# Optimization experiments

Measured on AMD Instinct MI355X. Metric: run time of the kernel, lower is better.

The kernel has to match this reference:

```python
import jax, jax.numpy as jnp
import numpy as np

MAX_SIZE = 650   # hard-coded node count in the original module
HIDDEN = 512     # hidden_dim
BATCH = 512      # batch_size (conv4 out channels)
IN_DIM = 512
N_EDGES = 150000


def _segment_softmax(e, dst, n):
    # torch_geometric.utils.softmax over destination-node segments
    m = jax.ops.segment_max(e, dst, num_segments=n)
    ex = jnp.exp(e - m[dst])
    s = jax.ops.segment_sum(ex, dst, num_segments=n)
    return ex / (s[dst] + 1e-16)


def _gat_conv(x, src, dst, W, a_src, a_dst, b, n, neg_slope=0.2):
    # PyG GATConv, heads=1, edge_dim=None (edge_attr ignored)
    h = x @ W                            # [n, out]
    al_s = h @ a_src                     # [n] per-node source attention logit
    al_d = h @ a_dst                     # [n] per-node dest attention logit
    e = jax.nn.leaky_relu(al_s[src] + al_d[dst], neg_slope)   # [E]
    alpha = _segment_softmax(e, dst, n)                        # [E]
    out = jax.ops.segment_sum(alpha[:, None] * h[src], dst, num_segments=n)
    return out + b


def setup_inputs() -> dict:
    key = jax.random.key(0)
    ks = jax.random.split(key, 12)
    inp = {
        "x_s": jax.random.normal(ks[0], (400, IN_DIM), jnp.float32),
        "x_t": jax.random.normal(ks[1], (250, IN_DIM), jnp.float32),
        "edge_index": jax.random.randint(ks[2], (2, N_EDGES), 0, MAX_SIZE, dtype=jnp.int32),
        "distances": jax.random.uniform(ks[3], (N_EDGES,), jnp.float32),
        "batch": jnp.zeros((MAX_SIZE,), jnp.int32),
        "W1": jax.random.normal(ks[4], (IN_DIM, HIDDEN), jnp.float32) / np.sqrt(IN_DIM).astype(np.float32),
        "a_src1": jax.random.normal(ks[5], (HIDDEN,), jnp.float32) * 0.1,
        "a_dst1": jax.random.normal(ks[6], (HIDDEN,), jnp.float32) * 0.1,
        "b1": jnp.zeros((HIDDEN,), jnp.float32),
        "W4": jax.random.normal(ks[7], (HIDDEN, BATCH), jnp.float32) / np.sqrt(HIDDEN).astype(np.float32),
        "a_src4": jax.random.normal(ks[8], (BATCH,), jnp.float32) * 0.1,
        "a_dst4": jax.random.normal(ks[9], (BATCH,), jnp.float32) * 0.1,
        "b4": jnp.zeros((BATCH,), jnp.float32),
        "fc_w": jax.random.normal(ks[10], (1, MAX_SIZE), jnp.float32) / np.sqrt(MAX_SIZE).astype(np.float32),
        "fc_b": jnp.zeros((1,), jnp.float32),
    }
    return inp


def reference(x_s, x_t, edge_index, distances, batch,
              W1, a_src1, a_dst1, b1, W4, a_src4, a_dst4, b4, fc_w, fc_b):
    # distances (edge_attr) and batch are unpacked but unused, as in the
    # original (GATConv with edge_dim=None ignores edge_attr).
    x = jnp.concatenate([x_s, x_t], axis=0)
    pad_n = max(MAX_SIZE - x.shape[0], 0)
    x = jnp.pad(x, ((0, pad_n), (0, 0)))            # [650, IN_DIM]
    # add_self_loops=True (PyG GATConv default)
    loop = jnp.arange(MAX_SIZE, dtype=edge_index.dtype)
    src = jnp.concatenate([edge_index[0], loop])
    dst = jnp.concatenate([edge_index[1], loop])
    x = _gat_conv(x, src, dst, W1, a_src1, a_dst1, b1, MAX_SIZE)
    x = jax.nn.relu(x)
    x = _gat_conv(x, src, dst, W4, a_src4, a_dst4, b4, MAX_SIZE)
    x = jax.nn.leaky_relu(x, 0.01)                  # [650, BATCH]
    x = x.reshape(BATCH, MAX_SIZE)                  # torch .view semantics (no transpose)
    x = x @ fc_w.T + fc_b                           # [BATCH, 1]
    x = x.squeeze()[None, :]                        # [1, BATCH]
    return jax.nn.sigmoid(x)
```

## Files before the change

### kernel.cpp

```cpp
#include <hip/hip_runtime.h>
#include <math.h>

#define N_NODES 650
#define DIM     512
#define E_RAW   150000
#define E_TOT   150650

#define BM 32
#define BN 64
#define BK 32
#define KC 128
#define NZ (DIM / KC)
#define CH 1024

__global__ __launch_bounds__(256)
void gemm_hp(const float* __restrict__ A, const float* __restrict__ Axt,
             const float* __restrict__ B, float* __restrict__ P,
             int M, int a_mode) {
    __shared__ float Ast[BK][BM + 2];
    __shared__ float Bs[BK][BN];
    int t  = threadIdx.x;
    int tx = t & 15, ty = t >> 4;
    int row0 = blockIdx.y * BM, col0 = blockIdx.x * BN;
    int kbase = blockIdx.z * KC;
    float acc[2][4] = {};

    for (int kb = kbase; kb < kbase + KC; kb += BK) {
        {
            int m  = t >> 3;
            int kq = (t & 7) * 4;
            int gr = row0 + m, gk = kb + kq;
            float4 v = make_float4(0.f, 0.f, 0.f, 0.f);
            if (gr < M) {
                const float* rowp;
                if (a_mode == 1)
                    rowp = (gr < 400) ? (A + (size_t)gr * DIM) : (Axt + (size_t)(gr - 400) * DIM);
                else
                    rowp = A + (size_t)gr * DIM;
                v = *(const float4*)(rowp + gk);
            }
            Ast[kq + 0][m] = v.x;
            Ast[kq + 1][m] = v.y;
            Ast[kq + 2][m] = v.z;
            Ast[kq + 3][m] = v.w;
        }
        {
            int n4 = (t & 15) * 4;
            #pragma unroll
            for (int p = 0; p < 2; p++) {
                int kk = (t >> 4) + p * 16;
                *(float4*)&Bs[kk][n4] = *(const float4*)&B[(size_t)(kb + kk) * DIM + col0 + n4];
            }
        }
        __syncthreads();
        #pragma unroll
        for (int kk = 0; kk < BK; kk++) {
            float2 a2 = *(const float2*)&Ast[kk][ty * 2];
            float4 b4 = *(const float4*)&Bs[kk][tx * 4];
            acc[0][0] += a2.x * b4.x; acc[0][1] += a2.x * b4.y;
            acc[0][2] += a2.x * b4.z; acc[0][3] += a2.x * b4.w;
            acc[1][0] += a2.y * b4.x; acc[1][1] += a2.y * b4.y;
            acc[1][2] += a2.y * b4.z; acc[1][3] += a2.y * b4.w;
        }
        __syncthreads();
    }

    float* Cout = P + (size_t)blockIdx.z * N_NODES * DIM;
    int gc0 = col0 + tx * 4;
    #pragma unroll
    for (int i = 0; i < 2; i++) {
        int gr = row0 + ty * 2 + i;
        if (gr < M)
            *(float4*)&Cout[(size_t)gr * DIM + gc0] =
                make_float4(acc[i][0], acc[i][1], acc[i][2], acc[i][3]);
    }
}

__global__ __launch_bounds__(256)
void reduce_logits(const float* __restrict__ P,
                   const float* __restrict__ asrc, const float* __restrict__ adst,
                   float* __restrict__ h, float* __restrict__ als, float* __restrict__ ald) {
    __shared__ float red[8];
    const size_t S = (size_t)N_NODES * DIM;
    int r = blockIdx.x, t = threadIdx.x;
    size_t base = (size_t)r * DIM;
    float v0 = 0.f, v1 = 0.f;
    #pragma unroll
    for (int z = 0; z < NZ; z++) {
        v0 += P[z * S + base + t];
        v1 += P[z * S + base + t + 256];
    }
    h[base + t]       = v0;
    h[base + t + 256] = v1;
    float ps = v0 * asrc[t] + v1 * asrc[t + 256];
    float pd = v0 * adst[t] + v1 * adst[t + 256];
    #pragma unroll
    for (int o = 32; o > 0; o >>= 1) {
        ps += __shfl_down(ps, o);
        pd += __shfl_down(pd, o);
    }
    if ((t & 63) == 0) { red[t >> 6] = ps; red[4 + (t >> 6)] = pd; }
    __syncthreads();
    if (t == 0) als[r] = red[0] + red[1] + red[2] + red[3];
    if (t == 1) ald[r] = red[4] + red[5] + red[6] + red[7];
}

__global__ __launch_bounds__(256)
void hist_kernel(const int* __restrict__ ei, int* __restrict__ cnt) {
    __shared__ int h[N_NODES];
    for (int l = threadIdx.x; l < N_NODES; l += 256) h[l] = 0;
    __syncthreads();
    for (int i = blockIdx.x * 256 + threadIdx.x; i < E_TOT; i += gridDim.x * 256) {
        int d = (i < E_RAW) ? ei[E_RAW + i] : i - E_RAW;
        atomicAdd(&h[d], 1);
    }
    __syncthreads();
    for (int l = threadIdx.x; l < N_NODES; l += 256) {
        int v = h[l];
        if (v) atomicAdd(&cnt[l], v);
    }
}

__global__ __launch_bounds__(1024)
void scan_kernel(const int* __restrict__ cnt, int* __restrict__ rowptr,
                 int* __restrict__ cursor) {
    __shared__ int buf[1024];
    int t = threadIdx.x;
    buf[t] = (t < N_NODES) ? cnt[t] : 0;
    __syncthreads();
    #pragma unroll
    for (int o = 1; o < 1024; o <<= 1) {
        int v = (t >= o) ? buf[t - o] : 0;
        __syncthreads();
        buf[t] += v;
        __syncthreads();
    }
    if (t < N_NODES) {
        int excl = (t == 0) ? 0 : buf[t - 1];
        rowptr[t] = excl;
        cursor[t] = excl;
    }
    if (t == 0) rowptr[N_NODES] = buf[N_NODES - 1];
}

__global__ __launch_bounds__(256)
void scatter_kernel(const int* __restrict__ ei, int* __restrict__ cursor,
                    int* __restrict__ ssrc) {
    int i = blockIdx.x * 256 + threadIdx.x;
    if (i >= E_TOT) return;
    int s, d;
    if (i < E_RAW) { s = ei[i]; d = ei[E_RAW + i]; }
    else           { s = d = i - E_RAW; }
    int pos = atomicAdd(&cursor[d], 1);
    ssrc[pos] = s;
}

__global__ __launch_bounds__(256)
void spmm_kernel(const int* __restrict__ rowptr, const int* __restrict__ ssrc,
                 const float* __restrict__ als, const float* __restrict__ ald,
                 const float* __restrict__ h, const float* __restrict__ bias,
                 float slope, float* __restrict__ outm) {
    __shared__ int   sS[CH];
    __shared__ float sE[CH];
    __shared__ float red[4];
    int d = blockIdx.x;
    int t = threadIdx.x;
    int c = blockIdx.y * 256 + t;
    int r0 = rowptr[d], r1 = rowptr[d + 1];
    int deg = r1 - r0;
    float aldd = ald[d];
    float acc = 0.f, psum = 0.f;

    for (int cb = 0; cb < deg; cb += CH) {
        int n = min(CH, deg - cb);
        __syncthreads();
        for (int l = t; l < n; l += 256) {
            int s = ssrc[r0 + cb + l];
            float v = als[s] + aldd;
            v = v > 0.f ? v : 0.2f * v;
            float ex = __expf(v);
            sS[l] = s;
            sE[l] = ex;
            psum += ex;
        }
        __syncthreads();
        int e = 0;
        for (; e + 4 <= n; e += 4) {
            int   s0 = sS[e],   s1 = sS[e+1], s2 = sS[e+2], s3 = sS[e+3];
            float e0 = sE[e],   e1 = sE[e+1], e2 = sE[e+2], e3 = sE[e+3];
            float x0 = h[(size_t)s0 * DIM + c];
            float x1 = h[(size_t)s1 * DIM + c];
            float x2 = h[(size_t)s2 * DIM + c];
            float x3 = h[(size_t)s3 * DIM + c];
            acc += e0 * x0 + e1 * x1 + e2 * x2 + e3 * x3;
        }
        for (; e < n; e++)
            acc += sE[e] * h[(size_t)sS[e] * DIM + c];
    }

    #pragma unroll
    for (int o = 32; o > 0; o >>= 1) psum += __shfl_down(psum, o);
    if ((t & 63) == 0) red[t >> 6] = psum;
    __syncthreads();
    float sum = red[0] + red[1] + red[2] + red[3];
    float v = acc / (sum + 1e-16f) + bias[c];
    v = v > 0.f ? v : slope * v;
    outm[(size_t)d * DIM + c] = v;
}

__global__ void final_kernel(const float* __restrict__ o2,
                             const float* __restrict__ fcw,
                             const float* __restrict__ fcb,
                             float* __restrict__ out) {
    int b = blockIdx.x * 4 + (threadIdx.x >> 6);
    int lane = threadIdx.x & 63;
    if (b >= 512) return;
    float s = 0.f;
    for (int i = lane; i < N_NODES; i += 64)
        s += o2[b * N_NODES + i] * fcw[i];
    #pragma unroll
    for (int o = 32; o > 0; o >>= 1) s += __shfl_down(s, o);
    if (lane == 0) out[b] = 1.f / (1.f + expf(-(s + fcb[0])));
}

extern "C" void kernel_launch(void* const* d_in, const int* in_sizes, int n_in,
                              void* d_out, int out_size, void* d_ws, size_t ws_size,
                              hipStream_t stream) {
    const float* x_s   = (const float*)d_in[0];
    const float* x_t   = (const float*)d_in[1];
    const int*   ei    = (const int*)d_in[2];
    const float* W1    = (const float*)d_in[5];
    const float* asrc1 = (const float*)d_in[6];
    const float* adst1 = (const float*)d_in[7];
    const float* b1    = (const float*)d_in[8];
    const float* W4    = (const float*)d_in[9];
    const float* asrc4 = (const float*)d_in[10];
    const float* adst4 = (const float*)d_in[11];
    const float* b4    = (const float*)d_in[12];
    const float* fcw   = (const float*)d_in[13];
    const float* fcb   = (const float*)d_in[14];
    float* out = (float*)d_out;

    const size_t H_ELEMS = (size_t)N_NODES * DIM;
    float* ws = (float*)d_ws;
    int*   cnt    = (int*)ws;
    int*   rowptr = cnt + N_NODES;
    int*   cursor = rowptr + N_NODES + 1;
    int*   ssrc   = cursor + N_NODES;
    float* als1   = (float*)(ssrc + E_TOT);
    float* ald1   = als1 + N_NODES;
    float* als2   = ald1 + N_NODES;
    float* ald2   = als2 + N_NODES;
    float* P      = ald2 + N_NODES;
    float* h1     = P + (size_t)NZ * H_ELEMS;
    float* o1     = h1 + H_ELEMS;
    float* h2     = h1;
    float* o2     = o1;

    hipMemsetAsync(cnt, 0, N_NODES * sizeof(int), stream);

    dim3 gG(DIM / BN, (N_NODES + BM - 1) / BM, NZ);
    dim3 gS(N_NODES, 2);
    int eBlocks = (E_TOT + 255) / 256;

    hist_kernel<<<64, 256, 0, stream>>>(ei, cnt);
    scan_kernel<<<1, 1024, 0, stream>>>(cnt, rowptr, cursor);
    scatter_kernel<<<eBlocks, 256, 0, stream>>>(ei, cursor, ssrc);

    gemm_hp<<<gG, 256, 0, stream>>>(x_s, x_t, W1, P, N_NODES, 1);
    reduce_logits<<<N_NODES, 256, 0, stream>>>(P, asrc1, adst1, h1, als1, ald1);
    spmm_kernel<<<gS, 256, 0, stream>>>(rowptr, ssrc, als1, ald1, h1, b1, 0.0f, o1);

    gemm_hp<<<gG, 256, 0, stream>>>(o1, nullptr, W4, P, N_NODES, 0);
    reduce_logits<<<N_NODES, 256, 0, stream>>>(P, asrc4, adst4, h2, als2, ald2);
    spmm_kernel<<<gS, 256, 0, stream>>>(rowptr, ssrc, als2, ald2, h2, b4, 0.01f, o2);

    final_kernel<<<128, 256, 0, stream>>>(o2, fcw, fcb, out);
}
```

Baseline: 218.0 us.

## Use per-block edge counts and shared-memory cursors for CSR build; shrink GEMM row tile

The CSR construction now has each of 64 blocks build a private histogram over a contiguous edge range. A single scan kernel computes per-block base offsets, and the scatter pass uses shared-memory cursors instead of global atomics on 650 counters, which removes the memset and heavy global atomic contention. Separately, the GEMM row tile is halved so each thread computes one row instead of two, doubling the number of blocks for more parallelism at the cost of less register reuse. The scan kernel does serial loops of 64 per thread, and the scatter is limited to 64 blocks.

```diff
diff --git a/kernel.cpp b/kernel.cpp
--- a/kernel.cpp
+++ b/kernel.cpp
@@ -6,12 +6,13 @@
 #define E_RAW   150000
 #define E_TOT   150650
 
-#define BM 32
+#define BM 16
 #define BN 64
 #define BK 32
 #define KC 128
 #define NZ (DIM / KC)
 #define CH 1024
+#define NB 64
 
 __global__ __launch_bounds__(256)
 void gemm_hp(const float* __restrict__ A, const float* __restrict__ Axt,
@@ -23,13 +24,13 @@
     int tx = t & 15, ty = t >> 4;
     int row0 = blockIdx.y * BM, col0 = blockIdx.x * BN;
     int kbase = blockIdx.z * KC;
-    float acc[2][4] = {};
+    float acc[4] = {};
 
     for (int kb = kbase; kb < kbase + KC; kb += BK) {
-        {
+        if (t < 128) {
             int m  = t >> 3;
             int kq = (t & 7) * 4;
-            int gr = row0 + m, gk = kb + kq;
+            int gr = row0 + m;
             float4 v = make_float4(0.f, 0.f, 0.f, 0.f);
             if (gr < M) {
                 const float* rowp;
@@ -37,7 +38,7 @@
                     rowp = (gr < 400) ? (A + (size_t)gr * DIM) : (Axt + (size_t)(gr - 400) * DIM);
                 else
                     rowp = A + (size_t)gr * DIM;
-                v = *(const float4*)(rowp + gk);
+                v = *(const float4*)(rowp + kb + kq);
             }
             Ast[kq + 0][m] = v.x;
             Ast[kq + 1][m] = v.y;
@@ -46,34 +47,28 @@
         }
         {
             int n4 = (t & 15) * 4;
+            int kk = t >> 4;
             #pragma unroll
-            for (int p = 0; p < 2; p++) {
-                int kk = (t >> 4) + p * 16;
-                *(float4*)&Bs[kk][n4] = *(const float4*)&B[(size_t)(kb + kk) * DIM + col0 + n4];
-            }
+            for (int p = 0; p < 2; p++)
+                *(float4*)&Bs[kk + p * 16][n4] =
+                    *(const float4*)&B[(size_t)(kb + kk + p * 16) * DIM + col0 + n4];
         }
         __syncthreads();
         #pragma unroll
         for (int kk = 0; kk < BK; kk++) {
-            float2 a2 = *(const float2*)&Ast[kk][ty * 2];
+            float a = Ast[kk][ty];
             float4 b4 = *(const float4*)&Bs[kk][tx * 4];
-            acc[0][0] += a2.x * b4.x; acc[0][1] += a2.x * b4.y;
-            acc[0][2] += a2.x * b4.z; acc[0][3] += a2.x * b4.w;
-            acc[1][0] += a2.y * b4.x; acc[1][1] += a2.y * b4.y;
-            acc[1][2] += a2.y * b4.z; acc[1][3] += a2.y * b4.w;
+            acc[0] += a * b4.x; acc[1] += a * b4.y;
+            acc[2] += a * b4.z; acc[3] += a * b4.w;
         }
         __syncthreads();
     }
 
     float* Cout = P + (size_t)blockIdx.z * N_NODES * DIM;
-    int gc0 = col0 + tx * 4;
-    #pragma unroll
-    for (int i = 0; i < 2; i++) {
-        int gr = row0 + ty * 2 + i;
-        if (gr < M)
-            *(float4*)&Cout[(size_t)gr * DIM + gc0] =
-                make_float4(acc[i][0], acc[i][1], acc[i][2], acc[i][3]);
-    }
+    int gr = row0 + ty;
+    if (gr < M)
+        *(float4*)&Cout[(size_t)gr * DIM + col0 + tx * 4] =
+            make_float4(acc[0], acc[1], acc[2], acc[3]);
 }
 
 __global__ __launch_bounds__(256)
@@ -106,27 +101,31 @@
 }
 
 __global__ __launch_bounds__(256)
-void hist_kernel(const int* __restrict__ ei, int* __restrict__ cnt) {
+void count_kernel(const int* __restrict__ ei, int* __restrict__ cntb) {
     __shared__ int h[N_NODES];
     for (int l = threadIdx.x; l < N_NODES; l += 256) h[l] = 0;
     __syncthreads();
-    for (int i = blockIdx.x * 256 + threadIdx.x; i < E_TOT; i += gridDim.x * 256) {
+    int per = (E_TOT + NB - 1) / NB;
+    int e0 = blockIdx.x * per;
+    int e1 = min(e0 + per, E_TOT);
+    for (int i = e0 + threadIdx.x; i < e1; i += 256) {
         int d = (i < E_RAW) ? ei[E_RAW + i] : i - E_RAW;
         atomicAdd(&h[d], 1);
     }
     __syncthreads();
-    for (int l = threadIdx.x; l < N_NODES; l += 256) {
-        int v = h[l];
-        if (v) atomicAdd(&cnt[l], v);
-    }
+    for (int l = threadIdx.x; l < N_NODES; l += 256)
+        cntb[blockIdx.x * N_NODES + l] = h[l];
 }
 
 __global__ __launch_bounds__(1024)
-void scan_kernel(const int* __restrict__ cnt, int* __restrict__ rowptr,
-                 int* __restrict__ cursor) {
+void scanbase_kernel(const int* __restrict__ cntb, int* __restrict__ rowptr,
+                     int* __restrict__ baseb) {
     __shared__ int buf[1024];
     int t = threadIdx.x;
-    buf[t] = (t < N_NODES) ? cnt[t] : 0;
+    int tot = 0;
+    if (t < N_NODES)
+        for (int b = 0; b < NB; b++) tot += cntb[b * N_NODES + t];
+    buf[t] = (t < N_NODES) ? tot : 0;
     __syncthreads();
     #pragma unroll
     for (int o = 1; o < 1024; o <<= 1) {
@@ -136,23 +135,33 @@
         __syncthreads();
     }
     if (t < N_NODES) {
-        int excl = (t == 0) ? 0 : buf[t - 1];
-        rowptr[t] = excl;
-        cursor[t] = excl;
-    }
-    if (t == 0) rowptr[N_NODES] = buf[N_NODES - 1];
-}
-
-__global__ __launch_bounds__(256)
-void scatter_kernel(const int* __restrict__ ei, int* __restrict__ cursor,
-                    int* __restrict__ ssrc) {
-    int i = blockIdx.x * 256 + threadIdx.x;
-    if (i >= E_TOT) return;
-    int s, d;
-    if (i < E_RAW) { s = ei[i]; d = ei[E_RAW + i]; }
-    else           { s = d = i - E_RAW; }
-    int pos = atomicAdd(&cursor[d], 1);
-    ssrc[pos] = s;
+        int run = buf[t] - tot;
+        rowptr[t] = run;
+        for (int b = 0; b < NB; b++) {
+            baseb[b * N_NODES + t] = run;
+            run += cntb[b * N_NODES + t];
+        }
+    }
+    if (t == 0) rowptr[N_NODES] = E_TOT;
+}
+
+__global__ __launch_bounds__(256)
+void scatter2_kernel(const int* __restrict__ ei, const int* __restrict__ baseb,
+                     int* __restrict__ ssrc) {
+    __shared__ int lcur[N_NODES];
+    for (int l = threadIdx.x; l < N_NODES; l += 256)
+        lcur[l] = baseb[blockIdx.x * N_NODES + l];
+    __syncthreads();
+    int per = (E_TOT + NB - 1) / NB;
+    int e0 = blockIdx.x * per;
+    int e1 = min(e0 + per, E_TOT);
+    for (int i = e0 + threadIdx.x; i < e1; i += 256) {
+        int s, d;
+        if (i < E_RAW) { s = ei[i]; d = ei[E_RAW + i]; }
+        else           { s = d = i - E_RAW; }
+        int pos = atomicAdd(&lcur[d], 1);
+        ssrc[pos] = s;
+    }
 }
 
 __global__ __launch_bounds__(256)
@@ -243,10 +252,10 @@
 
     const size_t H_ELEMS = (size_t)N_NODES * DIM;
     float* ws = (float*)d_ws;
-    int*   cnt    = (int*)ws;
-    int*   rowptr = cnt + N_NODES;
-    int*   cursor = rowptr + N_NODES + 1;
-    int*   ssrc   = cursor + N_NODES;
+    int*   cntb   = (int*)ws;
+    int*   baseb  = cntb + NB * N_NODES;
+    int*   rowptr = baseb + NB * N_NODES;
+    int*   ssrc   = rowptr + N_NODES + 1;
     float* als1   = (float*)(ssrc + E_TOT);
     float* ald1   = als1 + N_NODES;
     float* als2   = ald1 + N_NODES;
@@ -257,15 +266,12 @@
     float* h2     = h1;
     float* o2     = o1;
 
-    hipMemsetAsync(cnt, 0, N_NODES * sizeof(int), stream);
-
     dim3 gG(DIM / BN, (N_NODES + BM - 1) / BM, NZ);
     dim3 gS(N_NODES, 2);
-    int eBlocks = (E_TOT + 255) / 256;
-
-    hist_kernel<<<64, 256, 0, stream>>>(ei, cnt);
-    scan_kernel<<<1, 1024, 0, stream>>>(cnt, rowptr, cursor);
-    scatter_kernel<<<eBlocks, 256, 0, stream>>>(ei, cursor, ssrc);
+
+    count_kernel<<<NB, 256, 0, stream>>>(ei, cntb);
+    scanbase_kernel<<<1, 1024, 0, stream>>>(cntb, rowptr, baseb);
+    scatter2_kernel<<<NB, 256, 0, stream>>>(ei, baseb, ssrc);
 
     gemm_hp<<<gG, 256, 0, stream>>>(x_s, x_t, W1, P, N_NODES, 1);
     reduce_logits<<<N_NODES, 256, 0, stream>>>(P, asrc1, adst1, h1, als1, ald1);
```

After: 189.1 us. 13.3% less time.
